# Kernel optimization log

Hardware: AMD Instinct MI355X
Metric: run time of the kernel (lower is better)

Reference implementation:

```python
import jax, jax.numpy as jnp
import numpy as np

B, S, E = 2, 2048, 1024
H = 16
HD = E // H           # 64
KD = 64               # k_dim
VD = 64               # v_dim
SCALE = 1.0 / np.float32(np.sqrt(KD))


def setup_inputs() -> dict:
    key = jax.random.key(0)
    ks = jax.random.split(key, 10)
    return {
        "x": jax.random.normal(ks[0], (B, S, E), dtype=jnp.float32),
        "mask": jax.random.uniform(ks[1], (S, S), dtype=jnp.float32),
        "Wq": jax.random.normal(ks[2], (HD, KD), dtype=jnp.float32) * 0.05,
        "bq": jax.random.normal(ks[3], (KD,), dtype=jnp.float32) * 0.05,
        "Wk": jax.random.normal(ks[4], (HD, KD), dtype=jnp.float32) * 0.05,
        "bk": jax.random.normal(ks[5], (KD,), dtype=jnp.float32) * 0.05,
        "Wv": jax.random.normal(ks[6], (HD, VD), dtype=jnp.float32) * 0.05,
        "bv": jax.random.normal(ks[7], (VD,), dtype=jnp.float32) * 0.05,
        "Wo": jax.random.normal(ks[8], (H * VD, E), dtype=jnp.float32) * 0.05,
        "bo": jax.random.normal(ks[9], (E,), dtype=jnp.float32) * 0.05,
    }


def reference(x, mask, Wq, bq, Wk, bk, Wv, bv, Wo, bo):
    b, s, e = x.shape
    # (B, S, E) -> (B, H, S, head_dim)
    xh = x.reshape(b, s, H, HD).transpose(0, 2, 1, 3)
    q = jnp.einsum('bhsd,dk->bhsk', xh, Wq) + bq   # (B,H,S,KD)
    k = jnp.einsum('bhsd,dk->bhsk', xh, Wk) + bk   # (B,H,S,KD)
    v = jnp.einsum('bhsd,dv->bhsv', xh, Wv) + bv   # (B,H,S,VD)
    sim = jnp.einsum('bhqk,bhsk->bhqs', q, k) * SCALE  # (B,H,S,S)
    sim = sim * mask[None, None, :, :]                  # multiplicative mask
    attn = jax.nn.softmax(sim, axis=-1)
    out = jnp.einsum('bhqs,bhsv->bhqv', attn, v)        # (B,H,S,VD)
    out = out.transpose(0, 2, 1, 3).reshape(b, s, H * VD)
    return out @ Wo + bo
```

## Files before the change

### kernel.cpp

```cpp
#include <hip/hip_runtime.h>
#include <hip/hip_bf16.h>

#define SS 2048
#define EE 1024
#define SCALE 0.125f
#define LOG2E 1.44269504088896f

typedef __attribute__((ext_vector_type(8))) short short8;
typedef __attribute__((ext_vector_type(4))) float float4v;
typedef __attribute__((ext_vector_type(4))) unsigned int uint4v;

__device__ __forceinline__ unsigned short f2bf(float f) {
  unsigned int u = __float_as_uint(f);
  unsigned int lsb = (u >> 16) & 1u;
  u += 0x7fffu + lsb;
  return (unsigned short)(u >> 16);
}
__device__ __forceinline__ unsigned int pk2bf(float a, float b) {
  __hip_bfloat162 h = __float22bfloat162_rn(float2{a, b});
  return *reinterpret_cast<unsigned int*>(&h);
}

__global__ __launch_bounds__(256) void prep_kernel(
    const float* __restrict__ mask,
    const float* __restrict__ Wq, const float* __restrict__ Wk,
    const float* __restrict__ Wv,
    unsigned short* __restrict__ maskP, unsigned short* __restrict__ W3T)
{
  __shared__ unsigned short t[64 * 65];
  int blk = blockIdx.x;
  int tid = threadIdx.x;
  if (blk < 2048) {
    int idx = blk * 256 + tid;
    int lane = idx & 63, step = (idx >> 6) & 63, qt = idx >> 12;
    int li = lane & 15, g = lane >> 4;
    const float c = SCALE * LOG2E;
    const float* mrow = mask + (size_t)(qt * 16 + li) * SS + step * 32 + g * 4;
    float4 a = *(const float4*)mrow;
    float4 bb = *(const float4*)(mrow + 16);
    uint4v o;
    o.x = pk2bf(a.x * c, a.y * c);
    o.y = pk2bf(a.z * c, a.w * c);
    o.z = pk2bf(bb.x * c, bb.y * c);
    o.w = pk2bf(bb.z * c, bb.w * c);
    *(uint4v*)(maskP + (size_t)idx * 8) = o;
    return;
  }
  int m = blk - 2048;
  const float* W = (m == 0) ? Wq : (m == 1 ? Wk : Wv);
#pragma unroll
  for (int i = 0; i < 16; ++i) {
    int e = tid + i * 256; int d = e >> 6, n = e & 63;
    t[n * 65 + d] = f2bf(W[e]);
  }
  __syncthreads();
  unsigned short* dst = W3T + m * 4096;
#pragma unroll
  for (int i = 0; i < 16; ++i) {
    int e = tid + i * 256; int n = e >> 6, d = e & 63;
    dst[n * 64 + d] = t[n * 65 + d];
  }
}

__global__ __launch_bounds__(256) void qkv_kernel(
    const float* __restrict__ x, const unsigned short* __restrict__ W3T,
    const float* __restrict__ bq, const float* __restrict__ bk,
    const float* __restrict__ bv,
    unsigned short* __restrict__ Q, unsigned short* __restrict__ Kp,
    unsigned short* __restrict__ Vf)
{
  __shared__ __align__(16) unsigned short w3t[192 * 72];
  __shared__ __align__(16) unsigned short xt[64 * 72];
  __shared__ float sBias[192];
  int tid = threadIdx.x;
  int bh = blockIdx.x >> 4;
  int s0blk = (blockIdx.x & 15) * 128;
  int b = bh >> 4, h = bh & 15;
  int wv = tid >> 6, lane = tid & 63;
  int li = lane & 15, g = lane >> 4;

#pragma unroll
  for (int i = 0; i < 6; ++i) {
    int slot = tid + i * 256;
    int row = slot >> 3, c = slot & 7;
    *(short8*)(w3t + row * 72 + c * 8) = *(const short8*)(W3T + slot * 8);
  }
  if (tid < 192) sBias[tid] = (tid < 64) ? bq[tid] : (tid < 128 ? bk[tid - 64] : bv[tid - 128]);

  for (int half = 0; half < 2; ++half) {
    int s0 = s0blk + half * 64;
    if (half) __syncthreads();
    const float* xbase = x + ((size_t)(b * SS + s0)) * EE + h * 64;
#pragma unroll
    for (int it = 0; it < 4; ++it) {
      int flat = tid + it * 256;
      int row = flat >> 4, ch = flat & 15;
      float4 v = *(const float4*)(xbase + (size_t)row * EE + ch * 4);
      uint2 u; u.x = pk2bf(v.x, v.y); u.y = pk2bf(v.z, v.w);
      *(uint2*)(xt + row * 72 + ch * 4) = u;
    }
    __syncthreads();

    int mrow = wv * 16;
    short8 af[2];
#pragma unroll
    for (int ks = 0; ks < 2; ++ks)
      af[ks] = *(const short8*)(xt + (mrow + li) * 72 + ks * 32 + g * 8);

    float4v acc[12];
#pragma unroll
    for (int i = 0; i < 12; ++i) acc[i] = (float4v){0, 0, 0, 0};
#pragma unroll
    for (int ks = 0; ks < 2; ++ks)
#pragma unroll
      for (int nb = 0; nb < 12; ++nb) {
        short8 bfr = *(const short8*)(w3t + (nb * 16 + li) * 72 + ks * 32 + g * 8);
        acc[nb] = __builtin_amdgcn_mfma_f32_16x16x32_bf16(af[ks], bfr, acc[nb], 0, 0, 0);
      }

    int srow0 = s0 + mrow + g * 4;
#pragma unroll
    for (int nb = 0; nb < 12; ++nb) {
      float bias = sBias[nb * 16 + li];
      int mtx = nb >> 2, sub = nb & 3;
#pragma unroll
      for (int r = 0; r < 4; ++r) {
        unsigned short ob = f2bf(acc[nb][r] + bias);
        int s = srow0 + r;
        int step = s >> 5;
        if (mtx == 0) {
          Q[((size_t)bh * SS + s) * 64 + sub * 16 + li] = ob;
        } else if (mtx == 1) {
          int sb = (s >> 4) & 1, lik = s & 15;
          int part = sub >> 1;
          int gk = ((sub & 1) << 1) | (li >> 3);
          Kp[(size_t)bh * 131072 + step * 2048 + (sb * 2 + part) * 512 +
             (gk * 16 + lik) * 8 + (li & 7)] = ob;
        } else {
          int sl = s & 31;
          int pos = ((sl >> 2) & 3) * 8 + ((sl >> 4) & 1) * 4 + (sl & 3);
          Vf[(size_t)bh * 131072 + step * 2048 + sub * 512 +
             ((pos >> 3) * 16 + li) * 8 + (pos & 7)] = ob;
        }
      }
    }
  }
}

__global__ __launch_bounds__(256) void attn_kernel(
    const unsigned short* __restrict__ Q, const unsigned short* __restrict__ Kp,
    const unsigned short* __restrict__ Vf, const unsigned short* __restrict__ maskP,
    unsigned short* __restrict__ AO)
{
  __shared__ __align__(16) unsigned short lds[8192];
  int tid = threadIdx.x, wv = tid >> 6, lane = tid & 63;
  int li = lane & 15, g = lane >> 4;
  int bh = blockIdx.x >> 5;
  int q0 = (blockIdx.x & 31) * 64 + wv * 16;

  const unsigned short* Qb = Q + ((size_t)bh * SS + q0 + li) * 64;
  short8 qf0 = *(const short8*)(Qb + g * 8);
  short8 qf1 = *(const short8*)(Qb + 32 + g * 8);

  const unsigned short* Kg = Kp + (size_t)bh * 131072 + tid * 8;
  const unsigned short* Vg = Vf + (size_t)bh * 131072 + tid * 8;
  const unsigned short* Mg = maskP + (size_t)(q0 >> 4) * 32768 + lane * 8;

  unsigned short ov = (li == 0) ? (unsigned short)0x3F80 : (unsigned short)0;
  short8 vones = {(short)ov, (short)ov, (short)ov, (short)ov,
                  (short)ov, (short)ov, (short)ov, (short)ov};

  float4v acc[4];
#pragma unroll
  for (int nb = 0; nb < 4; ++nb) acc[nb] = (float4v){0, 0, 0, 0};
  float4v accd = {0, 0, 0, 0};

  short8 kreg = *(const short8*)Kg;
  short8 vreg = *(const short8*)Vg;
  uint4v mc = *(const uint4v*)Mg;
  *(short8*)(lds + tid * 8) = kreg;
  *(short8*)(lds + 2048 + tid * 8) = vreg;
  __syncthreads();

  for (int step = 0; step < 64; ++step) {
    const unsigned short* ktc = lds + ((step & 1) ? 4096 : 0);
    const unsigned short* vtc = ktc + 2048;
    unsigned short* ktn = lds + ((step & 1) ? 0 : 4096);
    unsigned short* vtn = ktn + 2048;
    int ns = (step + 1) & 63;
    kreg = *(const short8*)(Kg + (size_t)ns * 2048);
    vreg = *(const short8*)(Vg + (size_t)ns * 2048);
    uint4v mn = *(const uint4v*)(Mg + (size_t)ns * 512);

    short8 kf00 = *(const short8*)(ktc + lane * 8);
    short8 kf01 = *(const short8*)(ktc + 512 + lane * 8);
    short8 kf10 = *(const short8*)(ktc + 1024 + lane * 8);
    short8 kf11 = *(const short8*)(ktc + 1536 + lane * 8);

    uint4v pw;
    {
      float4v st = {0, 0, 0, 0};
      st = __builtin_amdgcn_mfma_f32_16x16x32_bf16(kf00, qf0, st, 0, 0, 0);
      st = __builtin_amdgcn_mfma_f32_16x16x32_bf16(kf01, qf1, st, 0, 0, 0);
#pragma unroll
      for (int hh = 0; hh < 2; ++hh) {
        unsigned int mm = mc[hh];
        float p0 = __builtin_amdgcn_exp2f(st[2 * hh] * __uint_as_float(mm << 16));
        float p1 = __builtin_amdgcn_exp2f(st[2 * hh + 1] * __uint_as_float(mm & 0xffff0000u));
        pw[hh] = pk2bf(p0, p1);
      }
    }
    {
      float4v st = {0, 0, 0, 0};
      st = __builtin_amdgcn_mfma_f32_16x16x32_bf16(kf10, qf0, st, 0, 0, 0);
      st = __builtin_amdgcn_mfma_f32_16x16x32_bf16(kf11, qf1, st, 0, 0, 0);
#pragma unroll
      for (int hh = 0; hh < 2; ++hh) {
        unsigned int mm = mc[2 + hh];
        float p0 = __builtin_amdgcn_exp2f(st[2 * hh] * __uint_as_float(mm << 16));
        float p1 = __builtin_amdgcn_exp2f(st[2 * hh + 1] * __uint_as_float(mm & 0xffff0000u));
        pw[2 + hh] = pk2bf(p0, p1);
      }
    }
    short8 pf = *(short8*)&pw;
#pragma unroll
    for (int nb = 0; nb < 4; ++nb) {
      short8 vfr = *(const short8*)(vtc + nb * 512 + lane * 8);
      acc[nb] = __builtin_amdgcn_mfma_f32_16x16x32_bf16(vfr, pf, acc[nb], 0, 0, 0);
    }
    accd = __builtin_amdgcn_mfma_f32_16x16x32_bf16(vones, pf, accd, 0, 0, 0);

    *(short8*)(ktn + tid * 8) = kreg;
    *(short8*)(vtn + tid * 8) = vreg;
    mc = mn;
    __syncthreads();
  }

  float den = __shfl(accd[0], li, 64);
  float rd = 1.0f / den;

  unsigned short* tr = lds + wv * 1152;
#pragma unroll
  for (int nb = 0; nb < 4; ++nb) {
    int base = li * 72 + nb * 16 + g * 4;
    *(unsigned int*)(tr + base)     = pk2bf(acc[nb][0] * rd, acc[nb][1] * rd);
    *(unsigned int*)(tr + base + 2) = pk2bf(acc[nb][2] * rd, acc[nb][3] * rd);
  }
  asm volatile("s_waitcnt lgkmcnt(0)" ::: "memory");

  int b = bh >> 4, h = bh & 15;
  int rrow = lane >> 3, part = lane & 7;
#pragma unroll
  for (int i = 0; i < 2; ++i) {
    int row = i * 8 + rrow;
    short8 o = *(const short8*)(tr + row * 72 + part * 8);
    *(short8*)(AO + ((size_t)(b * SS + q0 + row)) * EE + h * 64 + part * 8) = o;
  }
}

__global__ __launch_bounds__(256) void transpose_wo(
    const float* __restrict__ Wo, unsigned short* __restrict__ WoT)
{
  __shared__ unsigned short t[64 * 65];
  int tid = threadIdx.x;
  int k0 = (blockIdx.x >> 4) * 64;
  int n0 = (blockIdx.x & 15) * 64;
#pragma unroll
  for (int i = 0; i < 16; ++i) {
    int idx = tid + i * 256;
    int k = idx >> 6, n = idx & 63;
    t[n * 65 + k] = f2bf(Wo[(size_t)(k0 + k) * 1024 + n0 + n]);
  }
  __syncthreads();
#pragma unroll
  for (int i = 0; i < 16; ++i) {
    int idx = tid + i * 256;
    int n = idx >> 6, k = idx & 63;
    WoT[(size_t)(n0 + n) * 1024 + k0 + k] = t[n * 65 + k];
  }
}

__global__ __launch_bounds__(256) void out_gemm(
    const unsigned short* __restrict__ AO, const unsigned short* __restrict__ WoT,
    const float* __restrict__ bo, float* __restrict__ out)
{
  __shared__ __align__(16) unsigned short at[128 * 72];
  __shared__ __align__(16) unsigned short bt[64 * 72];
  int tid = threadIdx.x, wv = tid >> 6, lane = tid & 63;
  int li = lane & 15, g = lane >> 4;
  int m0 = (blockIdx.x >> 4) * 128;
  int n0 = (blockIdx.x & 15) * 64;
  int wm = (wv & 1) * 64, wn = (wv >> 1) * 32;

  const unsigned short* Ag = AO + (size_t)m0 * 1024;
  const unsigned short* Bg = WoT + (size_t)n0 * 1024;
  int srow = tid >> 3, scol = (tid & 7) * 8;

  short8 apre[4], bpre[2];
  auto ldst = [&](int k0) {
#pragma unroll
    for (int i = 0; i < 4; ++i)
      apre[i] = *(const short8*)(Ag + (size_t)(srow + i * 32) * 1024 + k0 + scol);
#pragma unroll
    for (int i = 0; i < 2; ++i)
      bpre[i] = *(const short8*)(Bg + (size_t)(srow + i * 32) * 1024 + k0 + scol);
  };

  float4v acc[4][2];
#pragma unroll
  for (int mt = 0; mt < 4; ++mt)
#pragma unroll
    for (int nt = 0; nt < 2; ++nt) acc[mt][nt] = (float4v){0, 0, 0, 0};

  ldst(0);
  for (int k0 = 0; k0 < 1024; k0 += 64) {
    __syncthreads();
#pragma unroll
    for (int i = 0; i < 4; ++i)
      *(short8*)(at + (srow + i * 32) * 72 + scol) = apre[i];
#pragma unroll
    for (int i = 0; i < 2; ++i)
      *(short8*)(bt + (srow + i * 32) * 72 + scol) = bpre[i];
    int nk = (k0 + 64 < 1024) ? k0 + 64 : 0;
    ldst(nk);
    __syncthreads();
#pragma unroll
    for (int ks = 0; ks < 2; ++ks) {
      short8 afr[4], bfr[2];
#pragma unroll
      for (int mt = 0; mt < 4; ++mt)
        afr[mt] = *(const short8*)(at + (wm + mt * 16 + li) * 72 + ks * 32 + g * 8);
#pragma unroll
      for (int nt = 0; nt < 2; ++nt)
        bfr[nt] = *(const short8*)(bt + (wn + nt * 16 + li) * 72 + ks * 32 + g * 8);
#pragma unroll
      for (int mt = 0; mt < 4; ++mt)
#pragma unroll
        for (int nt = 0; nt < 2; ++nt)
          acc[mt][nt] = __builtin_amdgcn_mfma_f32_16x16x32_bf16(afr[mt], bfr[nt], acc[mt][nt], 0, 0, 0);
    }
  }
#pragma unroll
  for (int nt = 0; nt < 2; ++nt) {
    float bof = bo[n0 + wn + nt * 16 + li];
#pragma unroll
    for (int mt = 0; mt < 4; ++mt)
#pragma unroll
      for (int r = 0; r < 4; ++r)
        out[(size_t)(m0 + wm + mt * 16 + g * 4 + r) * 1024 + n0 + wn + nt * 16 + li] =
            acc[mt][nt][r] + bof;
  }
}

extern "C" void kernel_launch(void* const* d_in, const int* in_sizes, int n_in,
                              void* d_out, int out_size, void* d_ws, size_t ws_size,
                              hipStream_t stream) {
  const float* x    = (const float*)d_in[0];
  const float* mask = (const float*)d_in[1];
  const float* Wq   = (const float*)d_in[2];
  const float* bq   = (const float*)d_in[3];
  const float* Wk   = (const float*)d_in[4];
  const float* bk   = (const float*)d_in[5];
  const float* Wv   = (const float*)d_in[6];
  const float* bv   = (const float*)d_in[7];
  const float* Wo   = (const float*)d_in[8];
  const float* bo   = (const float*)d_in[9];
  float* out = (float*)d_out;

  unsigned short* ws = (unsigned short*)d_ws;
  unsigned short* Q     = ws;
  unsigned short* Kp    = ws + 4194304;
  unsigned short* Vf    = ws + 8388608;
  unsigned short* AO    = ws + 12582912;
  unsigned short* maskP = ws + 16777216;
  unsigned short* W3T = AO;
  unsigned short* WoT = maskP;

  prep_kernel<<<2051, 256, 0, stream>>>(mask, Wq, Wk, Wv, maskP, W3T);
  qkv_kernel<<<512, 256, 0, stream>>>(x, W3T, bq, bk, bv, Q, Kp, Vf);
  attn_kernel<<<1024, 256, 0, stream>>>(Q, Kp, Vf, maskP, AO);
  transpose_wo<<<256, 256, 0, stream>>>(Wo, WoT);
  out_gemm<<<512, 256, 0, stream>>>(AO, WoT, bo, out);
}
```

Measured before the change: 189.9 us.

## Stage QKV stores in LDS, register-stream K/V per wave, fuse Wo conversion into GEMM

The QKV kernel now stages its bf16 outputs in shared memory and writes Q, K and V with coalesced 16-byte stores instead of scattered 2-byte global stores. The attention kernel drops the shared-memory double buffer and barriers: each wave handles 32 query rows (two 16-row tiles) and streams K/V fragments directly from global memory into registers, reusing each K/V fragment across both tiles. The separate Wo transpose kernel is removed, and out_gemm now loads fp32 Wo directly and converts and transposes it into LDS. The trade-offs are more register pressure in attention, uncoalesced scalar LDS writes for B in the GEMM, and repeated Wo conversion in every block.

```diff
diff --git a/kernel.cpp b/kernel.cpp
--- a/kernel.cpp
+++ b/kernel.cpp
@@ -71,6 +71,7 @@
 {
   __shared__ __align__(16) unsigned short w3t[192 * 72];
   __shared__ __align__(16) unsigned short xt[64 * 72];
+  __shared__ __align__(16) unsigned short ob[12288];
   __shared__ float sBias[192];
   int tid = threadIdx.x;
   int bh = blockIdx.x >> 4;
@@ -118,31 +119,40 @@
         acc[nb] = __builtin_amdgcn_mfma_f32_16x16x32_bf16(af[ks], bfr, acc[nb], 0, 0, 0);
       }
 
-    int srow0 = s0 + mrow + g * 4;
 #pragma unroll
     for (int nb = 0; nb < 12; ++nb) {
       float bias = sBias[nb * 16 + li];
       int mtx = nb >> 2, sub = nb & 3;
 #pragma unroll
       for (int r = 0; r < 4; ++r) {
-        unsigned short ob = f2bf(acc[nb][r] + bias);
-        int s = srow0 + r;
-        int step = s >> 5;
+        unsigned short v = f2bf(acc[nb][r] + bias);
+        int sl = mrow + g * 4 + r;
+        int stp = sl >> 5, s5 = sl & 31;
         if (mtx == 0) {
-          Q[((size_t)bh * SS + s) * 64 + sub * 16 + li] = ob;
+          ob[sl * 64 + sub * 16 + li] = v;
         } else if (mtx == 1) {
-          int sb = (s >> 4) & 1, lik = s & 15;
+          int sb = s5 >> 4, lik = s5 & 15;
           int part = sub >> 1;
           int gk = ((sub & 1) << 1) | (li >> 3);
-          Kp[(size_t)bh * 131072 + step * 2048 + (sb * 2 + part) * 512 +
-             (gk * 16 + lik) * 8 + (li & 7)] = ob;
+          ob[4096 + stp * 2048 + (sb * 2 + part) * 512 + (gk * 16 + lik) * 8 + (li & 7)] = v;
         } else {
-          int sl = s & 31;
-          int pos = ((sl >> 2) & 3) * 8 + ((sl >> 4) & 1) * 4 + (sl & 3);
-          Vf[(size_t)bh * 131072 + step * 2048 + sub * 512 +
-             ((pos >> 3) * 16 + li) * 8 + (pos & 7)] = ob;
+          int pos = ((s5 >> 2) & 3) * 8 + ((s5 >> 4) & 1) * 4 + (s5 & 3);
+          ob[8192 + stp * 2048 + sub * 512 + ((pos >> 3) * 16 + li) * 8 + (pos & 7)] = v;
         }
       }
+    }
+    __syncthreads();
+
+    unsigned short* Qg = Q + ((size_t)bh * SS + s0) * 64;
+    unsigned short* Kg = Kp + (size_t)bh * 131072 + (s0 >> 5) * 2048;
+    unsigned short* Vg = Vf + (size_t)bh * 131072 + (s0 >> 5) * 2048;
+#pragma unroll
+    for (int i = 0; i < 6; ++i) {
+      int slot = tid + i * 256;
+      int rgn = slot >> 9, off = (slot & 511) * 8;
+      short8 v = *(const short8*)(ob + rgn * 4096 + off);
+      unsigned short* dst = (rgn == 0) ? (Qg + off) : (rgn == 1 ? (Kg + off) : (Vg + off));
+      *(short8*)dst = v;
     }
   }
 }
@@ -152,136 +162,114 @@
     const unsigned short* __restrict__ Vf, const unsigned short* __restrict__ maskP,
     unsigned short* __restrict__ AO)
 {
-  __shared__ __align__(16) unsigned short lds[8192];
+  __shared__ __align__(16) unsigned short tr_all[4 * 32 * 72];
   int tid = threadIdx.x, wv = tid >> 6, lane = tid & 63;
   int li = lane & 15, g = lane >> 4;
-  int bh = blockIdx.x >> 5;
-  int q0 = (blockIdx.x & 31) * 64 + wv * 16;
-
-  const unsigned short* Qb = Q + ((size_t)bh * SS + q0 + li) * 64;
-  short8 qf0 = *(const short8*)(Qb + g * 8);
-  short8 qf1 = *(const short8*)(Qb + 32 + g * 8);
-
-  const unsigned short* Kg = Kp + (size_t)bh * 131072 + tid * 8;
-  const unsigned short* Vg = Vf + (size_t)bh * 131072 + tid * 8;
-  const unsigned short* Mg = maskP + (size_t)(q0 >> 4) * 32768 + lane * 8;
+  int wave_id = blockIdx.x * 4 + wv;
+  int bh = wave_id >> 6;
+  int q0 = (wave_id & 63) * 32;
+
+  short8 qf[2][2];
+#pragma unroll
+  for (int t = 0; t < 2; ++t) {
+    const unsigned short* Qb = Q + ((size_t)bh * SS + q0 + t * 16 + li) * 64;
+    qf[t][0] = *(const short8*)(Qb + g * 8);
+    qf[t][1] = *(const short8*)(Qb + 32 + g * 8);
+  }
+
+  const unsigned short* Kg = Kp + (size_t)bh * 131072 + lane * 8;
+  const unsigned short* Vg = Vf + (size_t)bh * 131072 + lane * 8;
+  const unsigned short* Mg0 = maskP + (size_t)(q0 >> 4) * 32768 + lane * 8;
+  const unsigned short* Mg1 = Mg0 + 32768;
 
   unsigned short ov = (li == 0) ? (unsigned short)0x3F80 : (unsigned short)0;
   short8 vones = {(short)ov, (short)ov, (short)ov, (short)ov,
                   (short)ov, (short)ov, (short)ov, (short)ov};
 
-  float4v acc[4];
-#pragma unroll
-  for (int nb = 0; nb < 4; ++nb) acc[nb] = (float4v){0, 0, 0, 0};
-  float4v accd = {0, 0, 0, 0};
-
-  short8 kreg = *(const short8*)Kg;
-  short8 vreg = *(const short8*)Vg;
-  uint4v mc = *(const uint4v*)Mg;
-  *(short8*)(lds + tid * 8) = kreg;
-  *(short8*)(lds + 2048 + tid * 8) = vreg;
-  __syncthreads();
+  float4v acc[2][4];
+#pragma unroll
+  for (int t = 0; t < 2; ++t)
+#pragma unroll
+    for (int nb = 0; nb < 4; ++nb) acc[t][nb] = (float4v){0, 0, 0, 0};
+  float4v accd[2] = {{0, 0, 0, 0}, {0, 0, 0, 0}};
+
+  short8 kf[4];
+#pragma unroll
+  for (int i = 0; i < 4; ++i) kf[i] = *(const short8*)(Kg + i * 512);
+  uint4v mc0 = *(const uint4v*)Mg0;
+  uint4v mc1 = *(const uint4v*)Mg1;
 
   for (int step = 0; step < 64; ++step) {
-    const unsigned short* ktc = lds + ((step & 1) ? 4096 : 0);
-    const unsigned short* vtc = ktc + 2048;
-    unsigned short* ktn = lds + ((step & 1) ? 0 : 4096);
-    unsigned short* vtn = ktn + 2048;
     int ns = (step + 1) & 63;
-    kreg = *(const short8*)(Kg + (size_t)ns * 2048);
-    vreg = *(const short8*)(Vg + (size_t)ns * 2048);
-    uint4v mn = *(const uint4v*)(Mg + (size_t)ns * 512);
-
-    short8 kf00 = *(const short8*)(ktc + lane * 8);
-    short8 kf01 = *(const short8*)(ktc + 512 + lane * 8);
-    short8 kf10 = *(const short8*)(ktc + 1024 + lane * 8);
-    short8 kf11 = *(const short8*)(ktc + 1536 + lane * 8);
-
-    uint4v pw;
-    {
-      float4v st = {0, 0, 0, 0};
-      st = __builtin_amdgcn_mfma_f32_16x16x32_bf16(kf00, qf0, st, 0, 0, 0);
-      st = __builtin_amdgcn_mfma_f32_16x16x32_bf16(kf01, qf1, st, 0, 0, 0);
-#pragma unroll
-      for (int hh = 0; hh < 2; ++hh) {
-        unsigned int mm = mc[hh];
-        float p0 = __builtin_amdgcn_exp2f(st[2 * hh] * __uint_as_float(mm << 16));
-        float p1 = __builtin_amdgcn_exp2f(st[2 * hh + 1] * __uint_as_float(mm & 0xffff0000u));
-        pw[hh] = pk2bf(p0, p1);
+    short8 vf[4];
+#pragma unroll
+    for (int i = 0; i < 4; ++i)
+      vf[i] = *(const short8*)(Vg + (size_t)step * 2048 + i * 512);
+    short8 kn[4];
+#pragma unroll
+    for (int i = 0; i < 4; ++i)
+      kn[i] = *(const short8*)(Kg + (size_t)ns * 2048 + i * 512);
+    uint4v mn0 = *(const uint4v*)(Mg0 + (size_t)ns * 512);
+    uint4v mn1 = *(const uint4v*)(Mg1 + (size_t)ns * 512);
+
+    short8 pf[2];
+#pragma unroll
+    for (int t = 0; t < 2; ++t) {
+      uint4v pw;
+#pragma unroll
+      for (int sb = 0; sb < 2; ++sb) {
+        float4v st = {0, 0, 0, 0};
+        st = __builtin_amdgcn_mfma_f32_16x16x32_bf16(kf[sb * 2], qf[t][0], st, 0, 0, 0);
+        st = __builtin_amdgcn_mfma_f32_16x16x32_bf16(kf[sb * 2 + 1], qf[t][1], st, 0, 0, 0);
+#pragma unroll
+        for (int hh = 0; hh < 2; ++hh) {
+          unsigned int mm = (t == 0) ? mc0[sb * 2 + hh] : mc1[sb * 2 + hh];
+          float p0 = __builtin_amdgcn_exp2f(st[2 * hh] * __uint_as_float(mm << 16));
+          float p1 = __builtin_amdgcn_exp2f(st[2 * hh + 1] * __uint_as_float(mm & 0xffff0000u));
+          pw[sb * 2 + hh] = pk2bf(p0, p1);
+        }
       }
-    }
-    {
-      float4v st = {0, 0, 0, 0};
-      st = __builtin_amdgcn_mfma_f32_16x16x32_bf16(kf10, qf0, st, 0, 0, 0);
-      st = __builtin_amdgcn_mfma_f32_16x16x32_bf16(kf11, qf1, st, 0, 0, 0);
-#pragma unroll
-      for (int hh = 0; hh < 2; ++hh) {
-        unsigned int mm = mc[2 + hh];
-        float p0 = __builtin_amdgcn_exp2f(st[2 * hh] * __uint_as_float(mm << 16));
-        float p1 = __builtin_amdgcn_exp2f(st[2 * hh + 1] * __uint_as_float(mm & 0xffff0000u));
-        pw[2 + hh] = pk2bf(p0, p1);
-      }
-    }
-    short8 pf = *(short8*)&pw;
+      pf[t] = *(short8*)&pw;
+    }
 #pragma unroll
     for (int nb = 0; nb < 4; ++nb) {
-      short8 vfr = *(const short8*)(vtc + nb * 512 + lane * 8);
-      acc[nb] = __builtin_amdgcn_mfma_f32_16x16x32_bf16(vfr, pf, acc[nb], 0, 0, 0);
-    }
-    accd = __builtin_amdgcn_mfma_f32_16x16x32_bf16(vones, pf, accd, 0, 0, 0);
-
-    *(short8*)(ktn + tid * 8) = kreg;
-    *(short8*)(vtn + tid * 8) = vreg;
-    mc = mn;
-    __syncthreads();
-  }
-
-  float den = __shfl(accd[0], li, 64);
-  float rd = 1.0f / den;
-
-  unsigned short* tr = lds + wv * 1152;
-#pragma unroll
-  for (int nb = 0; nb < 4; ++nb) {
-    int base = li * 72 + nb * 16 + g * 4;
-    *(unsigned int*)(tr + base)     = pk2bf(acc[nb][0] * rd, acc[nb][1] * rd);
-    *(unsigned int*)(tr + base + 2) = pk2bf(acc[nb][2] * rd, acc[nb][3] * rd);
+      acc[0][nb] = __builtin_amdgcn_mfma_f32_16x16x32_bf16(vf[nb], pf[0], acc[0][nb], 0, 0, 0);
+      acc[1][nb] = __builtin_amdgcn_mfma_f32_16x16x32_bf16(vf[nb], pf[1], acc[1][nb], 0, 0, 0);
+    }
+    accd[0] = __builtin_amdgcn_mfma_f32_16x16x32_bf16(vones, pf[0], accd[0], 0, 0, 0);
+    accd[1] = __builtin_amdgcn_mfma_f32_16x16x32_bf16(vones, pf[1], accd[1], 0, 0, 0);
+
+#pragma unroll
+    for (int i = 0; i < 4; ++i) kf[i] = kn[i];
+    mc0 = mn0; mc1 = mn1;
+  }
+
+  unsigned short* tr = tr_all + wv * (32 * 72);
+#pragma unroll
+  for (int t = 0; t < 2; ++t) {
+    float den = __shfl(accd[t][0], li, 64);
+    float rd = 1.0f / den;
+#pragma unroll
+    for (int nb = 0; nb < 4; ++nb) {
+      int base = (t * 16 + li) * 72 + nb * 16 + g * 4;
+      *(unsigned int*)(tr + base)     = pk2bf(acc[t][nb][0] * rd, acc[t][nb][1] * rd);
+      *(unsigned int*)(tr + base + 2) = pk2bf(acc[t][nb][2] * rd, acc[t][nb][3] * rd);
+    }
   }
   asm volatile("s_waitcnt lgkmcnt(0)" ::: "memory");
 
   int b = bh >> 4, h = bh & 15;
   int rrow = lane >> 3, part = lane & 7;
 #pragma unroll
-  for (int i = 0; i < 2; ++i) {
+  for (int i = 0; i < 4; ++i) {
     int row = i * 8 + rrow;
     short8 o = *(const short8*)(tr + row * 72 + part * 8);
     *(short8*)(AO + ((size_t)(b * SS + q0 + row)) * EE + h * 64 + part * 8) = o;
   }
 }
 
-__global__ __launch_bounds__(256) void transpose_wo(
-    const float* __restrict__ Wo, unsigned short* __restrict__ WoT)
-{
-  __shared__ unsigned short t[64 * 65];
-  int tid = threadIdx.x;
-  int k0 = (blockIdx.x >> 4) * 64;
-  int n0 = (blockIdx.x & 15) * 64;
-#pragma unroll
-  for (int i = 0; i < 16; ++i) {
-    int idx = tid + i * 256;
-    int k = idx >> 6, n = idx & 63;
-    t[n * 65 + k] = f2bf(Wo[(size_t)(k0 + k) * 1024 + n0 + n]);
-  }
-  __syncthreads();
-#pragma unroll
-  for (int i = 0; i < 16; ++i) {
-    int idx = tid + i * 256;
-    int n = idx >> 6, k = idx & 63;
-    WoT[(size_t)(n0 + n) * 1024 + k0 + k] = t[n * 65 + k];
-  }
-}
-
 __global__ __launch_bounds__(256) void out_gemm(
-    const unsigned short* __restrict__ AO, const unsigned short* __restrict__ WoT,
+    const unsigned short* __restrict__ AO, const float* __restrict__ Wo,
     const float* __restrict__ bo, float* __restrict__ out)
 {
   __shared__ __align__(16) unsigned short at[128 * 72];
@@ -293,17 +281,19 @@
   int wm = (wv & 1) * 64, wn = (wv >> 1) * 32;
 
   const unsigned short* Ag = AO + (size_t)m0 * 1024;
-  const unsigned short* Bg = WoT + (size_t)n0 * 1024;
+  const float* Bg = Wo + n0;
   int srow = tid >> 3, scol = (tid & 7) * 8;
-
-  short8 apre[4], bpre[2];
+  int bkrow = tid >> 4, bch = tid & 15;
+
+  short8 apre[4];
+  float4 bpre[4];
   auto ldst = [&](int k0) {
 #pragma unroll
     for (int i = 0; i < 4; ++i)
       apre[i] = *(const short8*)(Ag + (size_t)(srow + i * 32) * 1024 + k0 + scol);
 #pragma unroll
-    for (int i = 0; i < 2; ++i)
-      bpre[i] = *(const short8*)(Bg + (size_t)(srow + i * 32) * 1024 + k0 + scol);
+    for (int i = 0; i < 4; ++i)
+      bpre[i] = *(const float4*)(Bg + (size_t)(k0 + bkrow + i * 16) * 1024 + bch * 4);
   };
 
   float4v acc[4][2];
@@ -319,8 +309,14 @@
     for (int i = 0; i < 4; ++i)
       *(short8*)(at + (srow + i * 32) * 72 + scol) = apre[i];
 #pragma unroll
-    for (int i = 0; i < 2; ++i)
-      *(short8*)(bt + (srow + i * 32) * 72 + scol) = bpre[i];
+    for (int i = 0; i < 4; ++i) {
+      int kr = bkrow + i * 16;
+      float4 v = bpre[i];
+      bt[(bch * 4 + 0) * 72 + kr] = f2bf(v.x);
+      bt[(bch * 4 + 1) * 72 + kr] = f2bf(v.y);
+      bt[(bch * 4 + 2) * 72 + kr] = f2bf(v.z);
+      bt[(bch * 4 + 3) * 72 + kr] = f2bf(v.w);
+    }
     int nk = (k0 + 64 < 1024) ? k0 + 64 : 0;
     ldst(nk);
     __syncthreads();
@@ -374,11 +370,9 @@
   unsigned short* AO    = ws + 12582912;
   unsigned short* maskP = ws + 16777216;
   unsigned short* W3T = AO;
-  unsigned short* WoT = maskP;
 
   prep_kernel<<<2051, 256, 0, stream>>>(mask, Wq, Wk, Wv, maskP, W3T);
   qkv_kernel<<<512, 256, 0, stream>>>(x, W3T, bq, bk, bv, Q, Kp, Vf);
-  attn_kernel<<<1024, 256, 0, stream>>>(Q, Kp, Vf, maskP, AO);
-  transpose_wo<<<256, 256, 0, stream>>>(Wo, WoT);
-  out_gemm<<<512, 256, 0, stream>>>(AO, WoT, bo, out);
-}
+  attn_kernel<<<512, 256, 0, stream>>>(Q, Kp, Vf, maskP, AO);
+  out_gemm<<<512, 256, 0, stream>>>(AO, Wo, bo, out);
+}
```

Measured after the change: 186.8 us. No clear change (-1.6%).
